# Optimization experiments

Measured on AMD Instinct MI355X. Metric: run time of the kernel, lower is better.

## Reference

```python
import jax, jax.numpy as jnp
import numpy as np

K_TOP = 8  # num_experts_per_tok


def setup_inputs() -> dict:
    key = jax.random.key(0)
    k1, k2, k3 = jax.random.split(key, 3)
    B, S, H, E = 4, 4096, 4096, 64
    hidden_states = jax.random.normal(k1, (B, S, H), dtype=jnp.float32)
    router_weight = jax.random.normal(k2, (E, H), dtype=jnp.float32)
    router_bias = jnp.zeros((E,), dtype=jnp.float32)
    expert_bias = jax.random.normal(k3, (E, H), dtype=jnp.float32) * 0.1
    return {
        "hidden_states": hidden_states,
        "router_weight": router_weight,
        "router_bias": router_bias,
        "expert_bias": expert_bias,
    }


def reference(hidden_states, router_weight, router_bias, expert_bias):
    B, S, H = hidden_states.shape
    E = router_weight.shape[0]
    T = B * S
    flat = hidden_states.reshape(T, H)                      # [T,H]
    logits = jnp.einsum("th,eh->te", flat, router_weight) + router_bias
    scores = jax.nn.softmax(logits, axis=-1)                # [T,E]
    topk_w, topk_idx = jax.lax.top_k(scores, K_TOP)         # [T,K]
    # combined[k,t] = flat[t] + expert_bias[topk_idx[t,k]]
    # output[t] = sum_k w[t,k] * combined[k,t]
    #           = flat[t]*sum_k w[t,k] + (scatter(w) @ expert_bias)[t]
    w_sum = topk_w.sum(axis=-1, keepdims=True)              # [T,1]
    w_dense = jnp.zeros((T, E), dtype=scores.dtype).at[
        jnp.arange(T)[:, None], topk_idx
    ].add(topk_w)                                           # [T,E] sparse->dense
    bias_mix = jnp.einsum("te,eh->th", w_dense, expert_bias)  # [T,H]
    out = flat * w_sum + bias_mix
    return out.reshape(B, S, H)
```

## Files before the change

kernel.cpp:

```cpp
#include <hip/hip_runtime.h>
#include <hip/hip_bf16.h>


typedef float f32x4 __attribute__((ext_vector_type(4)));
typedef short s16x8 __attribute__((ext_vector_type(8)));

#define HH 4096
#define EE 64
#define KTOP 8
#define TT 32
#define NT 256

__device__ __forceinline__ short f2bf(float x) {
  __hip_bfloat16 h = __float2bfloat16(x);
  return *reinterpret_cast<const short*>(&h);
}
__device__ __forceinline__ float bf2f(short s) {
  union { unsigned u; float f; } v;
  v.u = ((unsigned)(unsigned short)s) << 16;
  return v.f;
}

__device__ __forceinline__ void split8(const float4& a, const float4& b,
                                       s16x8& hi, s16x8& lo) {
  float x[8] = {a.x, a.y, a.z, a.w, b.x, b.y, b.z, b.w};
#pragma unroll
  for (int i = 0; i < 8; ++i) {
    short hb = f2bf(x[i]);
    float hf = bf2f(hb);
    short lb = f2bf(x[i] - hf);
    hi[i] = hb;
    lo[i] = lb;
  }
}

__global__ __launch_bounds__(NT, 2) void moe_router_combine(
    const float* __restrict__ flat,
    const float* __restrict__ rw,
    const float* __restrict__ rb,
    const float* __restrict__ eb,
    float* __restrict__ out) {
  __shared__ float lgP[4][TT][EE + 2];
  __shared__ float twS[TT][KTOP + 1];
  __shared__ int   tiS[TT][KTOP];

  const int tid  = threadIdx.x;
  const int lane = tid & 63;
  const int wv   = tid >> 6;
  const int lrow = lane & 15;
  const int lkg  = lane >> 4;
  const size_t t0 = (size_t)blockIdx.x * TT;

  f32x4 acc[2][4];
#pragma unroll
  for (int m = 0; m < 2; ++m)
#pragma unroll
    for (int e = 0; e < 4; ++e)
      acc[m][e] = (f32x4){0.f, 0.f, 0.f, 0.f};

  const int kbase = wv * (HH / 4) + lkg * 8;
  const float* pA0 = flat + (t0 + lrow) * HH + kbase;
  const float* pA1 = flat + (t0 + 16 + lrow) * HH + kbase;
  const float* pW  = rw + (size_t)lrow * HH + kbase;

  float4 a00, a01, a10, a11, w0[4], w1[4];
  {
    const int ko = 0;
    a00 = *(const float4*)(pA0 + ko);
    a01 = *(const float4*)(pA0 + ko + 4);
    a10 = *(const float4*)(pA1 + ko);
    a11 = *(const float4*)(pA1 + ko + 4);
#pragma unroll
    for (int et = 0; et < 4; ++et) {
      w0[et] = *(const float4*)(pW + (size_t)et * 16 * HH + ko);
      w1[et] = *(const float4*)(pW + (size_t)et * 16 * HH + ko + 4);
    }
  }

  for (int s = 0; s < 32; ++s) {
    s16x8 Ah0, Al0, Ah1, Al1, Wh[4], Wl[4];
    split8(a00, a01, Ah0, Al0);
    split8(a10, a11, Ah1, Al1);
#pragma unroll
    for (int et = 0; et < 4; ++et) split8(w0[et], w1[et], Wh[et], Wl[et]);

    if (s + 1 < 32) {
      const int ko = (s + 1) * 32;
      a00 = *(const float4*)(pA0 + ko);
      a01 = *(const float4*)(pA0 + ko + 4);
      a10 = *(const float4*)(pA1 + ko);
      a11 = *(const float4*)(pA1 + ko + 4);
#pragma unroll
      for (int et = 0; et < 4; ++et) {
        w0[et] = *(const float4*)(pW + (size_t)et * 16 * HH + ko);
        w1[et] = *(const float4*)(pW + (size_t)et * 16 * HH + ko + 4);
      }
    }

#pragma unroll
    for (int et = 0; et < 4; ++et) {
      acc[0][et] = __builtin_amdgcn_mfma_f32_16x16x32_bf16(Ah0, Wh[et], acc[0][et], 0, 0, 0);
      acc[0][et] = __builtin_amdgcn_mfma_f32_16x16x32_bf16(Ah0, Wl[et], acc[0][et], 0, 0, 0);
      acc[0][et] = __builtin_amdgcn_mfma_f32_16x16x32_bf16(Al0, Wh[et], acc[0][et], 0, 0, 0);
      acc[1][et] = __builtin_amdgcn_mfma_f32_16x16x32_bf16(Ah1, Wh[et], acc[1][et], 0, 0, 0);
      acc[1][et] = __builtin_amdgcn_mfma_f32_16x16x32_bf16(Ah1, Wl[et], acc[1][et], 0, 0, 0);
      acc[1][et] = __builtin_amdgcn_mfma_f32_16x16x32_bf16(Al1, Wh[et], acc[1][et], 0, 0, 0);
    }
  }

#pragma unroll
  for (int mt = 0; mt < 2; ++mt)
#pragma unroll
    for (int et = 0; et < 4; ++et)
#pragma unroll
      for (int r = 0; r < 4; ++r)
        lgP[wv][mt * 16 + (lane >> 4) * 4 + r][et * 16 + (lane & 15)] = acc[mt][et][r];
  __syncthreads();

#pragma unroll
  for (int i = 0; i < (TT * EE) / NT; ++i) {
    int idx = tid + NT * i;
    int t = idx >> 6, e = idx & 63;
    float v = lgP[0][t][e] + lgP[1][t][e] + lgP[2][t][e] + lgP[3][t][e] + rb[e];
    lgP[0][t][e] = v;
  }
  __syncthreads();

  for (int i = 0; i < TT / 4; ++i) {
    const int tl = wv * (TT / 4) + i;
    float l = lgP[0][tl][lane];
    float m = l;
#pragma unroll
    for (int off = 32; off > 0; off >>= 1) m = fmaxf(m, __shfl_xor(m, off, 64));
    float p = __expf(l - m);
    float sum = p;
#pragma unroll
    for (int off = 32; off > 0; off >>= 1) sum += __shfl_xor(sum, off, 64);
    const float inv = 1.0f / sum;

    float cur = l;
    float wsum = 0.f;
    for (int k = 0; k < KTOP; ++k) {
      float v = cur;
      int a = lane;
#pragma unroll
      for (int off = 32; off > 0; off >>= 1) {
        float v2 = __shfl_xor(v, off, 64);
        int   a2 = __shfl_xor(a, off, 64);
        if (v2 > v || (v2 == v && a2 < a)) { v = v2; a = a2; }
      }
      float wk = __shfl(p, a, 64) * inv;
      wsum += wk;
      if (lane == 0) { twS[tl][k] = wk; tiS[tl][k] = a; }
      if (lane == a) cur = -1e30f;
    }
    if (lane == 0) twS[tl][KTOP] = wsum;
  }
  __syncthreads();

  const int HV = HH / 4;
  for (int i = 0; i < TT / 4; ++i) {
    const int tl = wv * (TT / 4) + i;
    const size_t tg = t0 + tl;
    const float wsm = twS[tl][KTOP];
    float wk[KTOP];
    const float4* ebp[KTOP];
#pragma unroll
    for (int k = 0; k < KTOP; ++k) {
      wk[k]  = twS[tl][k];
      ebp[k] = reinterpret_cast<const float4*>(eb + (size_t)tiS[tl][k] * HH);
    }
    const float4* fr   = reinterpret_cast<const float4*>(flat + tg * HH);
    float4*       orow = reinterpret_cast<float4*>(out + tg * HH);
#pragma unroll 2
    for (int h = lane; h < HV; h += 64) {
      float4 x = fr[h];
      float4 o;
      o.x = x.x * wsm; o.y = x.y * wsm; o.z = x.z * wsm; o.w = x.w * wsm;
#pragma unroll
      for (int k = 0; k < KTOP; ++k) {
        float4 b = ebp[k][h];
        o.x = fmaf(wk[k], b.x, o.x);
        o.y = fmaf(wk[k], b.y, o.y);
        o.z = fmaf(wk[k], b.z, o.z);
        o.w = fmaf(wk[k], b.w, o.w);
      }
      orow[h] = o;
    }
  }
}

extern "C" void kernel_launch(void* const* d_in, const int* in_sizes, int n_in,
                              void* d_out, int out_size, void* d_ws, size_t ws_size,
                              hipStream_t stream) {
  const float* flat = (const float*)d_in[0];
  const float* rw   = (const float*)d_in[1];
  const float* rb   = (const float*)d_in[2];
  const float* eb   = (const float*)d_in[3];
  float* out = (float*)d_out;

  const int T = in_sizes[0] / HH;
  const int nblk = T / TT;
  moe_router_combine<<<dim3(nblk), dim3(NT), 0, stream>>>(flat, rw, rb, eb, out);
}
```

Before: 645.1 us.

## Split fused router/combine kernel into presplit, router-topk, and streaming combine kernels

Replaces the single fused kernel with three launches. The first pre-splits router weights into bf16 hi/lo once. The second runs the router GEMM plus softmax/top-k on 16-token tiles and writes weights and indices to workspace. The third streams the combine with all 256 threads per token row. This removes the per-block weight splitting and gives each phase its own occupancy. In exchange it reads the hidden states twice (router and combine, which the fused kernel may have hit in cache) and depends on the workspace being large enough; otherwise it falls back to the fused kernel.

```diff
diff --git a/kernel.cpp b/kernel.cpp
--- a/kernel.cpp
+++ b/kernel.cpp
@@ -8,8 +8,13 @@
 #define HH 4096
 #define EE 64
 #define KTOP 8
-#define TT 32
-#define NT 256
+
+#define WS_WHI 0u
+#define WS_WLO (EE * HH * 2u)
+#define WS_TW  (WS_WLO + EE * HH * 2u)
+#define WS_TSUM(T) (WS_TW + (unsigned)(T) * 8u * 4u)
+#define WS_TIDX(T) (WS_TSUM(T) + (unsigned)(T) * 4u)
+#define WS_REQ(T)  (WS_TIDX(T) + (unsigned)(T) * 8u * 4u)
 
 __device__ __forceinline__ short f2bf(float x) {
   __hip_bfloat16 h = __float2bfloat16(x);
@@ -34,11 +39,168 @@
   }
 }
 
+__global__ __launch_bounds__(256) void prep_split(const float* __restrict__ rw,
+                                                  short* __restrict__ whi,
+                                                  short* __restrict__ wlo) {
+  const int i = blockIdx.x * blockDim.x + threadIdx.x;
+  const float4 a = reinterpret_cast<const float4*>(rw)[2 * i];
+  const float4 b = reinterpret_cast<const float4*>(rw)[2 * i + 1];
+  s16x8 hi, lo;
+  split8(a, b, hi, lo);
+  *reinterpret_cast<s16x8*>(whi + 8 * (size_t)i) = hi;
+  *reinterpret_cast<s16x8*>(wlo + 8 * (size_t)i) = lo;
+}
+
+__global__ __launch_bounds__(256, 4) void router_topk(
+    const float* __restrict__ flat, const short* __restrict__ whi,
+    const short* __restrict__ wlo, const float* __restrict__ rb,
+    float* __restrict__ tw, float* __restrict__ tsum, int* __restrict__ tidx) {
+  __shared__ float lg[4][16][EE + 2];
+
+  const int tid  = threadIdx.x;
+  const int lane = tid & 63;
+  const int wv   = tid >> 6;
+  const int lrow = lane & 15;
+  const int lkg  = lane >> 4;
+  const size_t t0 = (size_t)blockIdx.x * 16;
+
+  f32x4 acc[4];
+#pragma unroll
+  for (int e = 0; e < 4; ++e) acc[e] = (f32x4){0.f, 0.f, 0.f, 0.f};
+
+  const int kb = wv * (HH / 4) + lkg * 8;
+  const float* pA = flat + (t0 + lrow) * HH + kb;
+  const short* pH = whi + (size_t)lrow * HH + kb;
+  const short* pL = wlo + (size_t)lrow * HH + kb;
+
+  float4 a0, a1; s16x8 wh0, wh1, wh2, wh3, wl0, wl1, wl2, wl3;
+  a0 = *(const float4*)(pA);
+  a1 = *(const float4*)(pA + 4);
+  wh0 = *(const s16x8*)(pH + 0 * 16 * HH); wl0 = *(const s16x8*)(pL + 0 * 16 * HH);
+  wh1 = *(const s16x8*)(pH + 1 * 16 * HH); wl1 = *(const s16x8*)(pL + 1 * 16 * HH);
+  wh2 = *(const s16x8*)(pH + 2 * 16 * HH); wl2 = *(const s16x8*)(pL + 2 * 16 * HH);
+  wh3 = *(const s16x8*)(pH + 3 * 16 * HH); wl3 = *(const s16x8*)(pL + 3 * 16 * HH);
+
+  for (int s = 0; s < 32; ++s) {
+    s16x8 Ah, Al;
+    split8(a0, a1, Ah, Al);
+    s16x8 ch0 = wh0, ch1 = wh1, ch2 = wh2, ch3 = wh3;
+    s16x8 cl0 = wl0, cl1 = wl1, cl2 = wl2, cl3 = wl3;
+
+    if (s + 1 < 32) {
+      const int ko = (s + 1) * 32;
+      a0 = *(const float4*)(pA + ko);
+      a1 = *(const float4*)(pA + ko + 4);
+      wh0 = *(const s16x8*)(pH + 0 * 16 * HH + ko); wl0 = *(const s16x8*)(pL + 0 * 16 * HH + ko);
+      wh1 = *(const s16x8*)(pH + 1 * 16 * HH + ko); wl1 = *(const s16x8*)(pL + 1 * 16 * HH + ko);
+      wh2 = *(const s16x8*)(pH + 2 * 16 * HH + ko); wl2 = *(const s16x8*)(pL + 2 * 16 * HH + ko);
+      wh3 = *(const s16x8*)(pH + 3 * 16 * HH + ko); wl3 = *(const s16x8*)(pL + 3 * 16 * HH + ko);
+    }
+
+    acc[0] = __builtin_amdgcn_mfma_f32_16x16x32_bf16(Ah, ch0, acc[0], 0, 0, 0);
+    acc[0] = __builtin_amdgcn_mfma_f32_16x16x32_bf16(Ah, cl0, acc[0], 0, 0, 0);
+    acc[0] = __builtin_amdgcn_mfma_f32_16x16x32_bf16(Al, ch0, acc[0], 0, 0, 0);
+    acc[1] = __builtin_amdgcn_mfma_f32_16x16x32_bf16(Ah, ch1, acc[1], 0, 0, 0);
+    acc[1] = __builtin_amdgcn_mfma_f32_16x16x32_bf16(Ah, cl1, acc[1], 0, 0, 0);
+    acc[1] = __builtin_amdgcn_mfma_f32_16x16x32_bf16(Al, ch1, acc[1], 0, 0, 0);
+    acc[2] = __builtin_amdgcn_mfma_f32_16x16x32_bf16(Ah, ch2, acc[2], 0, 0, 0);
+    acc[2] = __builtin_amdgcn_mfma_f32_16x16x32_bf16(Ah, cl2, acc[2], 0, 0, 0);
+    acc[2] = __builtin_amdgcn_mfma_f32_16x16x32_bf16(Al, ch2, acc[2], 0, 0, 0);
+    acc[3] = __builtin_amdgcn_mfma_f32_16x16x32_bf16(Ah, ch3, acc[3], 0, 0, 0);
+    acc[3] = __builtin_amdgcn_mfma_f32_16x16x32_bf16(Ah, cl3, acc[3], 0, 0, 0);
+    acc[3] = __builtin_amdgcn_mfma_f32_16x16x32_bf16(Al, ch3, acc[3], 0, 0, 0);
+  }
+
+#pragma unroll
+  for (int e = 0; e < 4; ++e)
+#pragma unroll
+    for (int r = 0; r < 4; ++r)
+      lg[wv][(lane >> 4) * 4 + r][e * 16 + (lane & 15)] = acc[e][r];
+  __syncthreads();
+
+#pragma unroll
+  for (int i = 0; i < (16 * EE) / 256; ++i) {
+    int idx = tid + 256 * i;
+    int t = idx >> 6, e = idx & 63;
+    lg[0][t][e] = lg[0][t][e] + lg[1][t][e] + lg[2][t][e] + lg[3][t][e] + rb[e];
+  }
+  __syncthreads();
+
+  for (int i = 0; i < 4; ++i) {
+    const int tl = wv * 4 + i;
+    const size_t tg = t0 + tl;
+    float l = lg[0][tl][lane];
+    float m = l;
+#pragma unroll
+    for (int off = 32; off > 0; off >>= 1) m = fmaxf(m, __shfl_xor(m, off, 64));
+    float p = __expf(l - m);
+    float sum = p;
+#pragma unroll
+    for (int off = 32; off > 0; off >>= 1) sum += __shfl_xor(sum, off, 64);
+    const float inv = 1.0f / sum;
+
+    float cur = l;
+    float wsum = 0.f;
+    for (int k = 0; k < KTOP; ++k) {
+      float v = cur;
+      int a = lane;
+#pragma unroll
+      for (int off = 32; off > 0; off >>= 1) {
+        float v2 = __shfl_xor(v, off, 64);
+        int   a2 = __shfl_xor(a, off, 64);
+        if (v2 > v || (v2 == v && a2 < a)) { v = v2; a = a2; }
+      }
+      float wk = __shfl(p, a, 64) * inv;
+      wsum += wk;
+      if (lane == 0) { tw[tg * 8 + k] = wk; tidx[tg * 8 + k] = a; }
+      if (lane == a) cur = -1e30f;
+    }
+    if (lane == 0) tsum[tg] = wsum;
+  }
+}
+
+__global__ __launch_bounds__(256, 4) void combine_stream(
+    const float* __restrict__ flat, const float* __restrict__ eb,
+    const float* __restrict__ tw, const float* __restrict__ tsum,
+    const int* __restrict__ tidx, float* __restrict__ out) {
+  const int tid = threadIdx.x;
+  const int HV = HH / 4;
+  for (int it = 0; it < 8; ++it) {
+    const size_t t = (size_t)blockIdx.x * 8 + it;
+    const float wsm = tsum[t];
+    float wk[KTOP];
+    const float4* ebp[KTOP];
+#pragma unroll
+    for (int k = 0; k < KTOP; ++k) {
+      wk[k]  = tw[t * 8 + k];
+      ebp[k] = reinterpret_cast<const float4*>(eb + (size_t)tidx[t * 8 + k] * HH);
+    }
+    const float4* fr   = reinterpret_cast<const float4*>(flat + t * HH);
+    float4*       orow = reinterpret_cast<float4*>(out + t * HH);
+#pragma unroll
+    for (int i = 0; i < HV / 256; ++i) {
+      const int h = tid + i * 256;
+      float4 x = fr[h];
+      float4 o;
+      o.x = x.x * wsm; o.y = x.y * wsm; o.z = x.z * wsm; o.w = x.w * wsm;
+#pragma unroll
+      for (int k = 0; k < KTOP; ++k) {
+        float4 b = ebp[k][h];
+        o.x = fmaf(wk[k], b.x, o.x);
+        o.y = fmaf(wk[k], b.y, o.y);
+        o.z = fmaf(wk[k], b.z, o.z);
+        o.w = fmaf(wk[k], b.w, o.w);
+      }
+      orow[h] = o;
+    }
+  }
+}
+
+#define TT 32
+#define NT 256
 __global__ __launch_bounds__(NT, 2) void moe_router_combine(
-    const float* __restrict__ flat,
-    const float* __restrict__ rw,
-    const float* __restrict__ rb,
-    const float* __restrict__ eb,
+    const float* __restrict__ flat, const float* __restrict__ rw,
+    const float* __restrict__ rb, const float* __restrict__ eb,
     float* __restrict__ out) {
   __shared__ float lgP[4][TT][EE + 2];
   __shared__ float twS[TT][KTOP + 1];
@@ -55,8 +217,7 @@
 #pragma unroll
   for (int m = 0; m < 2; ++m)
 #pragma unroll
-    for (int e = 0; e < 4; ++e)
-      acc[m][e] = (f32x4){0.f, 0.f, 0.f, 0.f};
+    for (int e = 0; e < 4; ++e) acc[m][e] = (f32x4){0.f, 0.f, 0.f, 0.f};
 
   const int kbase = wv * (HH / 4) + lkg * 8;
   const float* pA0 = flat + (t0 + lrow) * HH + kbase;
@@ -64,17 +225,12 @@
   const float* pW  = rw + (size_t)lrow * HH + kbase;
 
   float4 a00, a01, a10, a11, w0[4], w1[4];
-  {
-    const int ko = 0;
-    a00 = *(const float4*)(pA0 + ko);
-    a01 = *(const float4*)(pA0 + ko + 4);
-    a10 = *(const float4*)(pA1 + ko);
-    a11 = *(const float4*)(pA1 + ko + 4);
-#pragma unroll
-    for (int et = 0; et < 4; ++et) {
-      w0[et] = *(const float4*)(pW + (size_t)et * 16 * HH + ko);
-      w1[et] = *(const float4*)(pW + (size_t)et * 16 * HH + ko + 4);
-    }
+  a00 = *(const float4*)(pA0); a01 = *(const float4*)(pA0 + 4);
+  a10 = *(const float4*)(pA1); a11 = *(const float4*)(pA1 + 4);
+#pragma unroll
+  for (int et = 0; et < 4; ++et) {
+    w0[et] = *(const float4*)(pW + (size_t)et * 16 * HH);
+    w1[et] = *(const float4*)(pW + (size_t)et * 16 * HH + 4);
   }
 
   for (int s = 0; s < 32; ++s) {
@@ -83,20 +239,16 @@
     split8(a10, a11, Ah1, Al1);
 #pragma unroll
     for (int et = 0; et < 4; ++et) split8(w0[et], w1[et], Wh[et], Wl[et]);
-
     if (s + 1 < 32) {
       const int ko = (s + 1) * 32;
-      a00 = *(const float4*)(pA0 + ko);
-      a01 = *(const float4*)(pA0 + ko + 4);
-      a10 = *(const float4*)(pA1 + ko);
-      a11 = *(const float4*)(pA1 + ko + 4);
+      a00 = *(const float4*)(pA0 + ko); a01 = *(const float4*)(pA0 + ko + 4);
+      a10 = *(const float4*)(pA1 + ko); a11 = *(const float4*)(pA1 + ko + 4);
 #pragma unroll
       for (int et = 0; et < 4; ++et) {
         w0[et] = *(const float4*)(pW + (size_t)et * 16 * HH + ko);
         w1[et] = *(const float4*)(pW + (size_t)et * 16 * HH + ko + 4);
       }
     }
-
 #pragma unroll
     for (int et = 0; et < 4; ++et) {
       acc[0][et] = __builtin_amdgcn_mfma_f32_16x16x32_bf16(Ah0, Wh[et], acc[0][et], 0, 0, 0);
@@ -107,7 +259,6 @@
       acc[1][et] = __builtin_amdgcn_mfma_f32_16x16x32_bf16(Al1, Wh[et], acc[1][et], 0, 0, 0);
     }
   }
-
 #pragma unroll
   for (int mt = 0; mt < 2; ++mt)
 #pragma unroll
@@ -116,16 +267,13 @@
       for (int r = 0; r < 4; ++r)
         lgP[wv][mt * 16 + (lane >> 4) * 4 + r][et * 16 + (lane & 15)] = acc[mt][et][r];
   __syncthreads();
-
 #pragma unroll
   for (int i = 0; i < (TT * EE) / NT; ++i) {
     int idx = tid + NT * i;
     int t = idx >> 6, e = idx & 63;
-    float v = lgP[0][t][e] + lgP[1][t][e] + lgP[2][t][e] + lgP[3][t][e] + rb[e];
-    lgP[0][t][e] = v;
-  }
-  __syncthreads();
-
+    lgP[0][t][e] = lgP[0][t][e] + lgP[1][t][e] + lgP[2][t][e] + lgP[3][t][e] + rb[e];
+  }
+  __syncthreads();
   for (int i = 0; i < TT / 4; ++i) {
     const int tl = wv * (TT / 4) + i;
     float l = lgP[0][tl][lane];
@@ -137,7 +285,6 @@
 #pragma unroll
     for (int off = 32; off > 0; off >>= 1) sum += __shfl_xor(sum, off, 64);
     const float inv = 1.0f / sum;
-
     float cur = l;
     float wsum = 0.f;
     for (int k = 0; k < KTOP; ++k) {
@@ -157,7 +304,6 @@
     if (lane == 0) twS[tl][KTOP] = wsum;
   }
   __syncthreads();
-
   const int HV = HH / 4;
   for (int i = 0; i < TT / 4; ++i) {
     const int tl = wv * (TT / 4) + i;
@@ -200,6 +346,19 @@
   float* out = (float*)d_out;
 
   const int T = in_sizes[0] / HH;
-  const int nblk = T / TT;
-  moe_router_combine<<<dim3(nblk), dim3(NT), 0, stream>>>(flat, rw, rb, eb, out);
-}
+
+  if (ws_size >= WS_REQ(T)) {
+    char* ws = (char*)d_ws;
+    short* whi  = (short*)(ws + WS_WHI);
+    short* wlo  = (short*)(ws + WS_WLO);
+    float* tw   = (float*)(ws + WS_TW);
+    float* tsum = (float*)(ws + WS_TSUM(T));
+    int*   tidx = (int*)(ws + WS_TIDX(T));
+
+    prep_split<<<dim3(EE * HH / 8 / 256), dim3(256), 0, stream>>>(rw, whi, wlo);
+    router_topk<<<dim3(T / 16), dim3(256), 0, stream>>>(flat, whi, wlo, rb, tw, tsum, tidx);
+    combine_stream<<<dim3(T / 8), dim3(256), 0, stream>>>(flat, eb, tw, tsum, tidx, out);
+  } else {
+    moe_router_combine<<<dim3(T / TT), dim3(NT), 0, stream>>>(flat, rw, rb, eb, out);
+  }
+}
```

Result: slower. 745.2 us (+15.5%).
